# Kernel tuning notes

Measured on AMD Instinct MI355X. Metric: run time of the kernel, lower is better.

## Reference

```python
import jax, jax.numpy as jnp
import numpy as np

N_NODES = 100000
N_EDGES = 3200000
IN_DIM, BIG, HID = 4, 32, 2
EPS = 1e-5


def _lin_init(key, fan_in, fan_out):
    # torch nn.Linear default: U(-1/sqrt(fan_in), 1/sqrt(fan_in))
    kw, kb = jax.random.split(key)
    bound = 1.0 / np.sqrt(fan_in)
    w = jax.random.uniform(kw, (fan_in, fan_out), minval=-bound, maxval=bound, dtype=jnp.float32)
    b = jax.random.uniform(kb, (fan_out,), minval=-bound, maxval=bound, dtype=jnp.float32)
    return w, b


def setup_inputs() -> dict:
    key = jax.random.key(0)
    ks = jax.random.split(key, 9)
    x = jax.random.normal(ks[0], (N_NODES, IN_DIM), dtype=jnp.float32)
    edge_index = jax.random.randint(ks[1], (2, N_EDGES), 0, N_NODES, dtype=jnp.int32)
    bn_w = jnp.ones((IN_DIM,), jnp.float32)
    bn_b = jnp.zeros((IN_DIM,), jnp.float32)
    enc_w1, enc_b1 = _lin_init(ks[2], 2 * IN_DIM, BIG)
    enc_w2, enc_b2 = _lin_init(ks[3], BIG, BIG)
    enc_w3, enc_b3 = _lin_init(ks[4], BIG, HID)
    dec_w1, dec_b1 = _lin_init(ks[5], 2 * HID, BIG)
    dec_w2, dec_b2 = _lin_init(ks[6], BIG, BIG)
    dec_w3, dec_b3 = _lin_init(ks[7], BIG, IN_DIM)
    return dict(x=x, edge_index=edge_index, bn_w=bn_w, bn_b=bn_b,
                enc_w1=enc_w1, enc_b1=enc_b1, enc_w2=enc_w2, enc_b2=enc_b2,
                enc_w3=enc_w3, enc_b3=enc_b3,
                dec_w1=dec_w1, dec_b1=dec_b1, dec_w2=dec_w2, dec_b2=dec_b2,
                dec_w3=dec_w3, dec_b3=dec_b3)


def _edge_conv(x, src, dst, w1, b1, w2, b2, w3, b3, final_relu):
    # PyG EdgeConv: message = nn(cat([x_i, x_j - x_i])), mean-aggregated at target i (=dst)
    xi = x[dst]                     # [E, F] gather (target)
    xj = x[src]                     # [E, F] gather (source)
    h = jnp.concatenate([xi, xj - xi], axis=-1)  # [E, 2F]
    h = jax.nn.relu(h @ w1 + b1)
    h = jax.nn.relu(h @ w2 + b2)
    h = h @ w3 + b3
    if final_relu:
        h = jax.nn.relu(h)
    n = x.shape[0]
    agg = jax.ops.segment_sum(h, dst, num_segments=n)          # [N, out]
    cnt = jax.ops.segment_sum(jnp.ones((h.shape[0],), h.dtype), dst, num_segments=n)
    return agg / jnp.maximum(cnt, 1.0)[:, None]


def reference(x, edge_index, bn_w, bn_b,
              enc_w1, enc_b1, enc_w2, enc_b2, enc_w3, enc_b3,
              dec_w1, dec_b1, dec_w2, dec_b2, dec_w3, dec_b3):
    # BatchNorm1d (training mode: batch statistics, biased variance)
    mu = jnp.mean(x, axis=0)
    var = jnp.var(x, axis=0)
    h = (x - mu) * jax.lax.rsqrt(var + EPS) * bn_w + bn_b
    src, dst = edge_index[0], edge_index[1]
    h = _edge_conv(h, src, dst, enc_w1, enc_b1, enc_w2, enc_b2, enc_w3, enc_b3, final_relu=True)
    h = _edge_conv(h, src, dst, dec_w1, dec_b1, dec_w2, dec_b2, dec_w3, dec_b3, final_relu=False)
    return h
```

## Files before the change

kernel.cpp:

```cpp
#include <hip/hip_runtime.h>

#define N_NODES 100000
#define N_EDGES 3200000
#define EPS 1e-5f
#define NODE_BLOCKS 391
#define NB 782
#define BSTRIDE 4608
#define NSUB 9
#define S1_EPB 8192
#define S1_BLOCKS 391

typedef unsigned int uint;
typedef uint u32x4 __attribute__((ext_vector_type(4)));
typedef _Float16 f16x8 __attribute__((ext_vector_type(8)));
typedef _Float16 f16x2 __attribute__((ext_vector_type(2)));
typedef float f32x16 __attribute__((ext_vector_type(16)));

static __device__ __forceinline__ f16x8 as_h8(u32x4 u) { return __builtin_bit_cast(f16x8, u); }
static __device__ __forceinline__ uint pkh(float a, float b) {
    return __builtin_bit_cast(uint, __builtin_amdgcn_cvt_pkrtz(a, b));
}
static __device__ __forceinline__ void swap32(uint& a, uint& b) {
    asm volatile("v_permlane32_swap_b32 %0, %1" : "+v"(a), "+v"(b));
}
static __device__ __forceinline__ uint prelu(uint u, uint z) {
    uint r;
    asm("v_pk_max_f16 %0, %1, %2" : "=v"(r) : "v"(u), "v"(z));
    return r;
}

#define MFMA(A, B, C) __builtin_amdgcn_mfma_f32_32x32x16_f16(as_h8(A), as_h8(B), (C), 0, 0, 0)

static __device__ __forceinline__ void repack(const f32x16& c, u32x4& f0, u32x4& f1, uint z) {
    uint p0 = prelu(pkh(c[0], c[1]), z),   p1 = prelu(pkh(c[2], c[3]), z);
    uint q0 = prelu(pkh(c[4], c[5]), z),   q1 = prelu(pkh(c[6], c[7]), z);
    uint p2 = prelu(pkh(c[8], c[9]), z),   p3 = prelu(pkh(c[10], c[11]), z);
    uint q2 = prelu(pkh(c[12], c[13]), z), q3 = prelu(pkh(c[14], c[15]), z);
    swap32(p0, q0); swap32(p1, q1);
    swap32(p2, q2); swap32(p3, q3);
    f0.x = p0; f0.y = p1; f0.z = q0; f0.w = q1;
    f1.x = p2; f1.y = p3; f1.z = q2; f1.w = q3;
}

#define OFF_STATS  0
#define OFF_BCNT   1024
#define OFF_INVCNT 5120
#define OFF_AGG1   405120
#define OFF_DECW   1205120
#define OFF_BUCKET 1214848
#define OFF_PENC   15629696
#define OFF_PCNT   22836608
#define OFF_PDEC   26440064
#define OFF_ENCW   26440064


__global__ __launch_bounds__(256) void k_bn_stats(const float* __restrict__ x,
                                                  double* __restrict__ stats) {
    int i = blockIdx.x * 256 + threadIdx.x;
    float4 v = make_float4(0.f, 0.f, 0.f, 0.f);
    if (i < N_NODES) v = ((const float4*)x)[i];
    double a[8];
    a[0] = v.x; a[1] = v.y; a[2] = v.z; a[3] = v.w;
    a[4] = (double)v.x * v.x; a[5] = (double)v.y * v.y;
    a[6] = (double)v.z * v.z; a[7] = (double)v.w * v.w;
    #pragma unroll
    for (int off = 32; off > 0; off >>= 1) {
        #pragma unroll
        for (int j = 0; j < 8; j++) a[j] += __shfl_down(a[j], off);
    }
    __shared__ double smem[4][8];
    int wave = threadIdx.x >> 6;
    int lane = threadIdx.x & 63;
    if (lane == 0) {
        #pragma unroll
        for (int j = 0; j < 8; j++) smem[wave][j] = a[j];
    }
    __syncthreads();
    if (threadIdx.x == 0) {
        #pragma unroll
        for (int j = 0; j < 8; j++) {
            double t = smem[0][j] + smem[1][j] + smem[2][j] + smem[3][j];
            atomicAdd(&stats[j], t);
        }
    }
}

static __device__ __forceinline__ uint pk_part(float a, float b, int part) {
    _Float16 ah = (_Float16)a, bh = (_Float16)b;
    if (part) {
        a -= (float)ah; b -= (float)bh;
        ah = (_Float16)a; bh = (_Float16)b;
    }
    return (uint)__builtin_bit_cast(unsigned short, ah) |
           ((uint)__builtin_bit_cast(unsigned short, bh) << 16);
}

__global__ __launch_bounds__(256) void k_prep(const double* __restrict__ stats,
                                              const float* __restrict__ bn_w,
                                              const float* __restrict__ bn_b,
                                              const float* __restrict__ ew1,
                                              const float* __restrict__ eb1,
                                              const float* __restrict__ ew2,
                                              const float* __restrict__ eb2,
                                              const float* __restrict__ ew3,
                                              const float* __restrict__ eb3,
                                              const float* __restrict__ dw1,
                                              const float* __restrict__ db1,
                                              const float* __restrict__ dw2,
                                              const float* __restrict__ db2,
                                              const float* __restrict__ dw3,
                                              const float* __restrict__ db3,
                                              uint* __restrict__ encw,
                                              uint* __restrict__ decw) {
    int t = threadIdx.x;
    int lane = t >> 2, d = t & 3;
    int hi = lane >> 5, m = lane & 31;

    const double inv_n = 1.0 / (double)N_NODES;
    float sc[4], sh[4];
    #pragma unroll
    for (int dd = 0; dd < 4; dd++) {
        double mu = stats[dd] * inv_n;
        double vr = stats[4 + dd] * inv_n - mu * mu;
        float rs = (float)(1.0 / sqrt(vr + (double)EPS));
        sc[dd] = rs * bn_w[dd];
        sh[dd] = bn_b[dd] - (float)mu * sc[dd];
    }

    {
        int j = 2 * d;
        float a = ew1[j * 32 + m] * sc[j & 3];
        float bb = ew1[(j + 1) * 32 + m] * sc[(j + 1) & 3];
        encw[t] = pk_part(a, bb, hi);
    }
    {
        int j = 2 * d;
        float a = (j < 4) ? dw1[j * 32 + m] : 0.f;
        float bb = (j + 1 < 4) ? dw1[(j + 1) * 32 + m] : 0.f;
        decw[t] = pk_part(a, bb, hi);
    }
    #pragma unroll
    for (int tile = 0; tile < 2; tile++) {
        int k = 16 * tile + 8 * hi + 2 * d;
        {
            float a = ew2[k * 32 + m], bb = ew2[(k + 1) * 32 + m];
            encw[256 + tile * 256 + t] = pk_part(a, bb, 0);
            encw[768 + tile * 256 + t] = pk_part(a, bb, 1);
        }
        {
            float a = dw2[k * 32 + m], bb = dw2[(k + 1) * 32 + m];
            decw[256 + tile * 256 + t] = pk_part(a, bb, 0);
            decw[768 + tile * 256 + t] = pk_part(a, bb, 1);
        }
        {
            float a = (m < 2) ? ew3[k * 2 + m] : 0.f;
            float bb = (m < 2) ? ew3[(k + 1) * 2 + m] : 0.f;
            encw[1280 + tile * 256 + t] = pk_part(a, bb, 0);
            encw[1792 + tile * 256 + t] = pk_part(a, bb, 1);
        }
        {
            float a = (m < 4) ? dw3[k * 4 + m] : 0.f;
            float bb = (m < 4) ? dw3[(k + 1) * 4 + m] : 0.f;
            decw[1280 + tile * 256 + t] = pk_part(a, bb, 0);
            decw[1792 + tile * 256 + t] = pk_part(a, bb, 1);
        }
    }
    if (t < 32) {
        int hh = t >> 4, r = t & 15;
        int row = (r & 3) + 8 * (r >> 2) + 4 * hh;
        float b1p = eb1[row];
        #pragma unroll
        for (int dd = 0; dd < 4; dd++) b1p += ew1[dd * 32 + row] * sh[dd];
        ((float*)encw)[2304 + t] = b1p;
        ((float*)encw)[2336 + t] = eb2[row];
        ((float*)encw)[2368 + t] = (row < 2) ? eb3[row] : 0.f;
        ((float*)decw)[2304 + t] = db1[row];
        ((float*)decw)[2336 + t] = db2[row];
        ((float*)decw)[2368 + t] = (row < 4) ? db3[row] : 0.f;
    }
}

__global__ __launch_bounds__(256) void k_s1(const int* __restrict__ ei,
                                            int* __restrict__ bcnt,
                                            int* __restrict__ bucket_buf) {
    __shared__ int hist[NB];
    __shared__ int base[NB];
    __shared__ int run[NB];
    __shared__ int gbase[NB];
    __shared__ int entries[S1_EPB];
    __shared__ unsigned short bk16[S1_EPB];
    __shared__ int wsum[4];
    int tid = threadIdx.x;
    int e0 = blockIdx.x * S1_EPB;
    for (int i = tid; i < NB; i += 256) hist[i] = 0;
    __syncthreads();
    #pragma unroll
    for (int k = 0; k < 32; k++) {
        int e = e0 + k * 256 + tid;
        if (e < N_EDGES) atomicAdd(&hist[ei[N_EDGES + e] >> 7], 1);
    }
    __syncthreads();
    int t4 = tid * 4;
    int h0 = (t4 + 0 < NB) ? hist[t4 + 0] : 0;
    int h1 = (t4 + 1 < NB) ? hist[t4 + 1] : 0;
    int h2 = (t4 + 2 < NB) ? hist[t4 + 2] : 0;
    int h3 = (t4 + 3 < NB) ? hist[t4 + 3] : 0;
    int tsum = h0 + h1 + h2 + h3;
    int lane = tid & 63, wv = tid >> 6;
    int xs = tsum;
    #pragma unroll
    for (int off = 1; off < 64; off <<= 1) {
        int u = __shfl_up(xs, off);
        if (lane >= off) xs += u;
    }
    if (lane == 63) wsum[wv] = xs;
    __syncthreads();
    int wo = 0;
    #pragma unroll
    for (int w = 0; w < 4; w++) if (w < wv) wo += wsum[w];
    int texcl = wo + xs - tsum;
    if (t4 + 0 < NB) base[t4 + 0] = texcl;
    if (t4 + 1 < NB) base[t4 + 1] = texcl + h0;
    if (t4 + 2 < NB) base[t4 + 2] = texcl + h0 + h1;
    if (t4 + 3 < NB) base[t4 + 3] = texcl + h0 + h1 + h2;
    __syncthreads();
    for (int i = tid; i < NB; i += 256) {
        int h = hist[i];
        gbase[i] = i * BSTRIDE + (h ? atomicAdd(&bcnt[i], h) : 0);
        run[i] = base[i];
    }
    __syncthreads();
    #pragma unroll
    for (int k = 0; k < 32; k++) {
        int e = e0 + k * 256 + tid;
        if (e < N_EDGES) {
            int s = ei[e];
            int d = ei[N_EDGES + e];
            int b = d >> 7;
            int r = atomicAdd(&run[b], 1);
            entries[r] = s | ((d & 127) << 17);
            bk16[r] = (unsigned short)b;
        }
    }
    __syncthreads();
    int nloc = min(S1_EPB, N_EDGES - e0);
    for (int idx = tid; idx < nloc; idx += 256) {
        int b = bk16[idx];
        bucket_buf[gbase[b] + (idx - base[b])] = entries[idx];
    }
}

__global__ __launch_bounds__(256, 3) void k_enc_partial(const float* __restrict__ x,
                                                        const int* __restrict__ bucket_buf,
                                                        const int* __restrict__ bcnt,
                                                        float2* __restrict__ penc,
                                                        int* __restrict__ pcnt,
                                                        const uint* __restrict__ encw) {
    __shared__ float4 xs[128];
    __shared__ float acc0[128], acc1[128];
    __shared__ int lc[128];
    int b = blockIdx.x, sub = blockIdx.y, tid = threadIdx.x;
    int lane = tid & 63, hi = lane >> 5, col = lane & 31, wv = tid >> 6;
    int cb = bcnt[b];
    int node0 = b << 7;

    if (tid < 128) {
        acc0[tid] = 0.f; acc1[tid] = 0.f; lc[tid] = 0;
        int n = node0 + tid;
        if (n >= N_NODES) n = 0;
        xs[tid] = ((const float4*)x)[n];
    }
    __syncthreads();

    const u32x4* W4 = (const u32x4*)encw;
    u32x4 w1   = W4[lane];
    u32x4 w2h0 = W4[64 + lane],  w2h1 = W4[128 + lane];
    u32x4 w2l0 = W4[192 + lane], w2l1 = W4[256 + lane];
    u32x4 u3h0 = W4[320 + lane], u3h1 = W4[384 + lane];
    u32x4 u3l0 = W4[448 + lane], u3l1 = W4[512 + lane];
    const float* tf = (const float*)encw;
    f32x16 b1f, b2f, b3f;
    {
        const float4* p1 = (const float4*)(tf + 2304 + hi * 16);
        const float4* p2 = (const float4*)(tf + 2336 + hi * 16);
        const float4* p3 = (const float4*)(tf + 2368 + hi * 16);
        #pragma unroll
        for (int q = 0; q < 4; q++) {
            float4 a = p1[q], c = p2[q], e = p3[q];
            b1f[4 * q] = a.x; b1f[4 * q + 1] = a.y; b1f[4 * q + 2] = a.z; b1f[4 * q + 3] = a.w;
            b2f[4 * q] = c.x; b2f[4 * q + 1] = c.y; b2f[4 * q + 2] = c.z; b2f[4 * q + 3] = c.w;
            b3f[4 * q] = e.x; b3f[4 * q + 1] = e.y; b3f[4 * q + 2] = e.z; b3f[4 * q + 3] = e.w;
        }
    }
    uint z = 0;

    if (sub * 512 < cb) {
        int sbase = sub * 512 + col * 16 + wv * 4;
        int4 q = *(const int4*)&bucket_buf[b * BSTRIDE + sbase];
        int ents[4] = {q.x, q.y, q.z, q.w};
        int ss[4], ia[4];
        #pragma unroll
        for (int t = 0; t < 4; t++) {
            int s = ents[t] & 0x1FFFF;
            if (s >= N_NODES) s = 0;
            ss[t] = s;
            ia[t] = (ents[t] >> 17) & 127;
        }
        float4 xj[4];
        #pragma unroll
        for (int t = 0; t < 4; t++) xj[t] = ((const float4*)x)[ss[t]];

        #pragma unroll
        for (int t = 0; t < 4; t++) {
            float4 xi = xs[ia[t]];
            u32x4 xf;
            xf.x = pkh(xi.x, xi.y);
            xf.y = pkh(xi.z, xi.w);
            xf.z = pkh(xj[t].x - xi.x, xj[t].y - xi.y);
            xf.w = pkh(xj[t].z - xi.z, xj[t].w - xi.w);
            f32x16 c = MFMA(w1, xf, b1f);
            u32x4 f0, f1;
            repack(c, f0, f1, z);
            f32x16 c2 = MFMA(w2h0, f0, b2f);
            c2 = MFMA(w2h1, f1, c2);
            c2 = MFMA(w2l0, f0, c2);
            c2 = MFMA(w2l1, f1, c2);
            u32x4 e0, e1;
            repack(c2, e0, e1, z);
            f32x16 c3 = MFMA(u3h0, e0, b3f);
            c3 = MFMA(u3h1, e1, c3);
            c3 = MFMA(u3l0, e0, c3);
            c3 = MFMA(u3l1, e1, c3);
            if (hi == 0 && (sbase + t) < cb) {
                float o0 = fmaxf(c3[0], 0.f);
                float o1 = fmaxf(c3[1], 0.f);
                atomicAdd(&acc0[ia[t]], o0);
                atomicAdd(&acc1[ia[t]], o1);
                atomicAdd(&lc[ia[t]], 1);
            }
        }
    }
    __syncthreads();
    if (tid < 128) {
        int pb = b * NSUB + sub;
        penc[pb * 128 + tid] = make_float2(acc0[tid], acc1[tid]);
        pcnt[pb * 128 + tid] = lc[tid];
    }
}

__global__ __launch_bounds__(256) void k_reduce_enc_p(const float2* __restrict__ penc,
                                                      const int* __restrict__ pcnt,
                                                      float2* __restrict__ agg1,
                                                      float* __restrict__ invcnt) {
    int i = blockIdx.x * 256 + threadIdx.x;
    if (i >= N_NODES) return;
    int b = i >> 7, l = i & 127;
    float a0 = 0.f, a1 = 0.f;
    int c = 0;
    #pragma unroll
    for (int sub = 0; sub < NSUB; sub++) {
        int idx = (b * NSUB + sub) * 128 + l;
        float2 p = penc[idx];
        a0 += p.x; a1 += p.y;
        c += pcnt[idx];
    }
    float ic = 1.0f / (float)(c > 1 ? c : 1);
    invcnt[i] = ic;
    agg1[i] = make_float2(a0 * ic, a1 * ic);
}

__global__ __launch_bounds__(256, 3) void k_dec_partial(const float2* __restrict__ henc,
                                                        const int* __restrict__ bucket_buf,
                                                        const int* __restrict__ bcnt,
                                                        float4* __restrict__ pdec,
                                                        const uint* __restrict__ decw) {
    __shared__ float2 hld[128];
    __shared__ float a0s[128], a1s[128], a2s[128], a3s[128];
    int b = blockIdx.x, sub = blockIdx.y, tid = threadIdx.x;
    int lane = tid & 63, hi = lane >> 5, col = lane & 31, wv = tid >> 6;
    int cb = bcnt[b];
    int node0 = b << 7;

    if (tid < 128) {
        a0s[tid] = 0.f; a1s[tid] = 0.f; a2s[tid] = 0.f; a3s[tid] = 0.f;
        int n = node0 + tid;
        if (n >= N_NODES) n = 0;
        hld[tid] = henc[n];
    }
    __syncthreads();

    const u32x4* W4 = (const u32x4*)decw;
    u32x4 v1   = W4[lane];
    u32x4 v2h0 = W4[64 + lane],  v2h1 = W4[128 + lane];
    u32x4 v2l0 = W4[192 + lane], v2l1 = W4[256 + lane];
    u32x4 u3h0 = W4[320 + lane], u3h1 = W4[384 + lane];
    u32x4 u3l0 = W4[448 + lane], u3l1 = W4[512 + lane];
    const float* tf = (const float*)decw;
    f32x16 b1f, b2f, b3f;
    {
        const float4* p1 = (const float4*)(tf + 2304 + hi * 16);
        const float4* p2 = (const float4*)(tf + 2336 + hi * 16);
        const float4* p3 = (const float4*)(tf + 2368 + hi * 16);
        #pragma unroll
        for (int q = 0; q < 4; q++) {
            float4 a = p1[q], c = p2[q], e = p3[q];
            b1f[4 * q] = a.x; b1f[4 * q + 1] = a.y; b1f[4 * q + 2] = a.z; b1f[4 * q + 3] = a.w;
            b2f[4 * q] = c.x; b2f[4 * q + 1] = c.y; b2f[4 * q + 2] = c.z; b2f[4 * q + 3] = c.w;
            b3f[4 * q] = e.x; b3f[4 * q + 1] = e.y; b3f[4 * q + 2] = e.z; b3f[4 * q + 3] = e.w;
        }
    }
    uint z = 0;

    if (sub * 512 < cb) {
        int sbase = sub * 512 + col * 16 + wv * 4;
        int4 q = *(const int4*)&bucket_buf[b * BSTRIDE + sbase];
        int ents[4] = {q.x, q.y, q.z, q.w};
        int ss[4], ia[4];
        #pragma unroll
        for (int t = 0; t < 4; t++) {
            int s = ents[t] & 0x1FFFF;
            if (s >= N_NODES) s = 0;
            ss[t] = s;
            ia[t] = (ents[t] >> 17) & 127;
        }
        float2 hj[4], hiv[4];
        #pragma unroll
        for (int t = 0; t < 4; t++) hj[t] = henc[ss[t]];
        #pragma unroll
        for (int t = 0; t < 4; t++) hiv[t] = hld[ia[t]];

        #pragma unroll
        for (int t = 0; t < 4; t++) {
            u32x4 xf;
            xf.x = pkh(hiv[t].x, hiv[t].y);
            xf.y = pkh(hj[t].x - hiv[t].x, hj[t].y - hiv[t].y);
            xf.z = 0u; xf.w = 0u;
            f32x16 c = MFMA(v1, xf, b1f);
            u32x4 f0, f1;
            repack(c, f0, f1, z);
            f32x16 c2 = MFMA(v2h0, f0, b2f);
            c2 = MFMA(v2h1, f1, c2);
            c2 = MFMA(v2l0, f0, c2);
            c2 = MFMA(v2l1, f1, c2);
            u32x4 e0, e1;
            repack(c2, e0, e1, z);
            f32x16 c3 = MFMA(u3h0, e0, b3f);
            c3 = MFMA(u3h1, e1, c3);
            c3 = MFMA(u3l0, e0, c3);
            c3 = MFMA(u3l1, e1, c3);
            if (hi == 0 && (sbase + t) < cb) {
                atomicAdd(&a0s[ia[t]], c3[0]);
                atomicAdd(&a1s[ia[t]], c3[1]);
                atomicAdd(&a2s[ia[t]], c3[2]);
                atomicAdd(&a3s[ia[t]], c3[3]);
            }
        }
    }
    __syncthreads();
    if (tid < 128) {
        int pb = b * NSUB + sub;
        pdec[pb * 128 + tid] = make_float4(a0s[tid], a1s[tid], a2s[tid], a3s[tid]);
    }
}

__global__ __launch_bounds__(256) void k_reduce_dec_p(const float4* __restrict__ pdec,
                                                      const float* __restrict__ invcnt,
                                                      float4* __restrict__ out) {
    int i = blockIdx.x * 256 + threadIdx.x;
    if (i >= N_NODES) return;
    int b = i >> 7, l = i & 127;
    float a0 = 0.f, a1 = 0.f, a2 = 0.f, a3 = 0.f;
    #pragma unroll
    for (int sub = 0; sub < NSUB; sub++) {
        float4 p = pdec[(b * NSUB + sub) * 128 + l];
        a0 += p.x; a1 += p.y; a2 += p.z; a3 += p.w;
    }
    float ic = invcnt[i];
    out[i] = make_float4(a0 * ic, a1 * ic, a2 * ic, a3 * ic);
}

extern "C" void kernel_launch(void* const* d_in, const int* in_sizes, int n_in,
                              void* d_out, int out_size, void* d_ws, size_t ws_size,
                              hipStream_t stream) {
    const float* x    = (const float*)d_in[0];
    const int*   ei   = (const int*)d_in[1];
    const float* bn_w = (const float*)d_in[2];
    const float* bn_b = (const float*)d_in[3];
    const float* ew1  = (const float*)d_in[4];
    const float* eb1  = (const float*)d_in[5];
    const float* ew2  = (const float*)d_in[6];
    const float* eb2  = (const float*)d_in[7];
    const float* ew3  = (const float*)d_in[8];
    const float* eb3  = (const float*)d_in[9];
    const float* dw1  = (const float*)d_in[10];
    const float* db1  = (const float*)d_in[11];
    const float* dw2  = (const float*)d_in[12];
    const float* db2  = (const float*)d_in[13];
    const float* dw3  = (const float*)d_in[14];
    const float* db3  = (const float*)d_in[15];

    char* ws = (char*)d_ws;
    double* stats      = (double*)(ws + OFF_STATS);
    int*    bcnt       = (int*)(ws + OFF_BCNT);
    float*  invcnt     = (float*)(ws + OFF_INVCNT);
    float2* agg1       = (float2*)(ws + OFF_AGG1);
    uint*   decw       = (uint*)(ws + OFF_DECW);
    int*    bucket_buf = (int*)(ws + OFF_BUCKET);
    float2* penc       = (float2*)(ws + OFF_PENC);
    int*    pcnt       = (int*)(ws + OFF_PCNT);
    float4* pdec       = (float4*)(ws + OFF_PDEC);
    uint*   encw       = (uint*)(ws + OFF_ENCW);
    float4* out        = (float4*)d_out;

    hipMemsetAsync(ws, 0, 5120, stream);

    k_bn_stats<<<NODE_BLOCKS, 256, 0, stream>>>(x, stats);
    k_prep<<<1, 256, 0, stream>>>(stats, bn_w, bn_b, ew1, eb1, ew2, eb2, ew3, eb3,
                                  dw1, db1, dw2, db2, dw3, db3, encw, decw);
    k_s1<<<S1_BLOCKS, 256, 0, stream>>>(ei, bcnt, bucket_buf);
    k_enc_partial<<<dim3(NB, NSUB), 256, 0, stream>>>(x, bucket_buf, bcnt,
                                                      penc, pcnt, encw);
    k_reduce_enc_p<<<NODE_BLOCKS, 256, 0, stream>>>(penc, pcnt, agg1, invcnt);
    k_dec_partial<<<dim3(NB, NSUB), 256, 0, stream>>>(agg1, bucket_buf, bcnt, pdec, decw);
    k_reduce_dec_p<<<NODE_BLOCKS, 256, 0, stream>>>(pdec, invcnt, out);
}
```

Before: 305.9 us.

## Halve layer-3 MFMAs via split output rows and process three edge windows per wave

Layer-3 weights are repacked so the output channels are spread across both half-waves, which cuts the final projection from four MFMAs to two per edge. Bias is folded in by subtracting b2 and adding a per-lane constant. Each half-wave now does its own atomics into separate accumulators. Sub-blocks drop from 9 to 3, and each wave handles three 512-edge windows, prefetching the next window's gathers before computing the current one, to hide gather latency and amortise block setup. The cost is fewer blocks in flight and more registers per thread.

```diff
diff --git a/kernel.cpp b/kernel.cpp
--- a/kernel.cpp
+++ b/kernel.cpp
@@ -6,14 +6,13 @@
 #define NODE_BLOCKS 391
 #define NB 782
 #define BSTRIDE 4608
-#define NSUB 9
+#define NSUB 3
 #define S1_EPB 8192
 #define S1_BLOCKS 391
 
 typedef unsigned int uint;
 typedef uint u32x4 __attribute__((ext_vector_type(4)));
 typedef _Float16 f16x8 __attribute__((ext_vector_type(8)));
-typedef _Float16 f16x2 __attribute__((ext_vector_type(2)));
 typedef float f32x16 __attribute__((ext_vector_type(16)));
 
 static __device__ __forceinline__ f16x8 as_h8(u32x4 u) { return __builtin_bit_cast(f16x8, u); }
@@ -40,6 +39,17 @@
     swap32(p2, q2); swap32(p3, q3);
     f0.x = p0; f0.y = p1; f0.z = q0; f0.w = q1;
     f1.x = p2; f1.y = p3; f1.z = q2; f1.w = q3;
+}
+
+static __device__ __forceinline__ void decode4(const int4& q, int* ss, int* ia) {
+    int e0 = q.x, e1 = q.y, e2 = q.z, e3 = q.w;
+    ss[0] = e0 & 0x1FFFF; ia[0] = (e0 >> 17) & 127;
+    ss[1] = e1 & 0x1FFFF; ia[1] = (e1 >> 17) & 127;
+    ss[2] = e2 & 0x1FFFF; ia[2] = (e2 >> 17) & 127;
+    ss[3] = e3 & 0x1FFFF; ia[3] = (e3 >> 17) & 127;
+    #pragma unroll
+    for (int k = 0; k < 4; k++)
+        if (ss[k] >= N_NODES) ss[k] = 0;
 }
 
 #define OFF_STATS  0
@@ -153,16 +163,20 @@
             decw[768 + tile * 256 + t] = pk_part(a, bb, 1);
         }
         {
-            float a = (m < 2) ? ew3[k * 2 + m] : 0.f;
-            float bb = (m < 2) ? ew3[(k + 1) * 2 + m] : 0.f;
+            float a = 0.f, bb = 0.f;
+            if (m == 0 || m == 4) {
+                int o = m >> 2;
+                a = ew3[k * 2 + o]; bb = ew3[(k + 1) * 2 + o];
+            }
             encw[1280 + tile * 256 + t] = pk_part(a, bb, 0);
-            encw[1792 + tile * 256 + t] = pk_part(a, bb, 1);
         }
         {
-            float a = (m < 4) ? dw3[k * 4 + m] : 0.f;
-            float bb = (m < 4) ? dw3[(k + 1) * 4 + m] : 0.f;
+            float a = 0.f, bb = 0.f;
+            if ((m & 3) < 2 && m < 6) {
+                int o = (m & 1) + 2 * (m >> 2);
+                a = dw3[k * 4 + o]; bb = dw3[(k + 1) * 4 + o];
+            }
             decw[1280 + tile * 256 + t] = pk_part(a, bb, 0);
-            decw[1792 + tile * 256 + t] = pk_part(a, bb, 1);
         }
     }
     if (t < 32) {
@@ -171,12 +185,13 @@
         float b1p = eb1[row];
         #pragma unroll
         for (int dd = 0; dd < 4; dd++) b1p += ew1[dd * 32 + row] * sh[dd];
-        ((float*)encw)[2304 + t] = b1p;
-        ((float*)encw)[2336 + t] = eb2[row];
-        ((float*)encw)[2368 + t] = (row < 2) ? eb3[row] : 0.f;
-        ((float*)decw)[2304 + t] = db1[row];
-        ((float*)decw)[2336 + t] = db2[row];
-        ((float*)decw)[2368 + t] = (row < 4) ? db3[row] : 0.f;
+        ((float*)encw)[1792 + t] = b1p;
+        ((float*)encw)[1824 + t] = eb2[row];
+        ((float*)encw)[1856 + t] = (row == 0) ? eb3[0] : (row == 4) ? eb3[1] : 0.f;
+        ((float*)decw)[1792 + t] = db1[row];
+        ((float*)decw)[1824 + t] = db2[row];
+        ((float*)decw)[1856 + t] =
+            ((row & 3) < 2 && row < 6) ? db3[(row & 1) + 2 * (row >> 2)] : 0.f;
     }
 }
 
@@ -276,69 +291,79 @@
     u32x4 w1   = W4[lane];
     u32x4 w2h0 = W4[64 + lane],  w2h1 = W4[128 + lane];
     u32x4 w2l0 = W4[192 + lane], w2l1 = W4[256 + lane];
-    u32x4 u3h0 = W4[320 + lane], u3h1 = W4[384 + lane];
-    u32x4 u3l0 = W4[448 + lane], u3l1 = W4[512 + lane];
+    u32x4 w30  = W4[320 + lane], w31  = W4[384 + lane];
     const float* tf = (const float*)encw;
-    f32x16 b1f, b2f, b3f;
+    f32x16 b1f, b2f;
     {
-        const float4* p1 = (const float4*)(tf + 2304 + hi * 16);
-        const float4* p2 = (const float4*)(tf + 2336 + hi * 16);
-        const float4* p3 = (const float4*)(tf + 2368 + hi * 16);
+        const float4* p1 = (const float4*)(tf + 1792 + hi * 16);
+        const float4* p2 = (const float4*)(tf + 1824 + hi * 16);
         #pragma unroll
         for (int q = 0; q < 4; q++) {
-            float4 a = p1[q], c = p2[q], e = p3[q];
+            float4 a = p1[q], c = p2[q];
             b1f[4 * q] = a.x; b1f[4 * q + 1] = a.y; b1f[4 * q + 2] = a.z; b1f[4 * q + 3] = a.w;
             b2f[4 * q] = c.x; b2f[4 * q + 1] = c.y; b2f[4 * q + 2] = c.z; b2f[4 * q + 3] = c.w;
-            b3f[4 * q] = e.x; b3f[4 * q + 1] = e.y; b3f[4 * q + 2] = e.z; b3f[4 * q + 3] = e.w;
-        }
-    }
+        }
+    }
+    float bc0 = tf[1856 + hi * 16] - b2f[0];
+    float* accH = hi ? acc1 : acc0;
     uint z = 0;
 
-    if (sub * 512 < cb) {
-        int sbase = sub * 512 + col * 16 + wv * 4;
-        int4 q = *(const int4*)&bucket_buf[b * BSTRIDE + sbase];
-        int ents[4] = {q.x, q.y, q.z, q.w};
-        int ss[4], ia[4];
-        #pragma unroll
-        for (int t = 0; t < 4; t++) {
-            int s = ents[t] & 0x1FFFF;
-            if (s >= N_NODES) s = 0;
-            ss[t] = s;
-            ia[t] = (ents[t] >> 17) & 127;
-        }
-        float4 xj[4];
-        #pragma unroll
-        for (int t = 0; t < 4; t++) xj[t] = ((const float4*)x)[ss[t]];
-
-        #pragma unroll
-        for (int t = 0; t < 4; t++) {
-            float4 xi = xs[ia[t]];
-            u32x4 xf;
-            xf.x = pkh(xi.x, xi.y);
-            xf.y = pkh(xi.z, xi.w);
-            xf.z = pkh(xj[t].x - xi.x, xj[t].y - xi.y);
-            xf.w = pkh(xj[t].z - xi.z, xj[t].w - xi.w);
-            f32x16 c = MFMA(w1, xf, b1f);
-            u32x4 f0, f1;
-            repack(c, f0, f1, z);
-            f32x16 c2 = MFMA(w2h0, f0, b2f);
-            c2 = MFMA(w2h1, f1, c2);
-            c2 = MFMA(w2l0, f0, c2);
-            c2 = MFMA(w2l1, f1, c2);
-            u32x4 e0, e1;
-            repack(c2, e0, e1, z);
-            f32x16 c3 = MFMA(u3h0, e0, b3f);
-            c3 = MFMA(u3h1, e1, c3);
-            c3 = MFMA(u3l0, e0, c3);
-            c3 = MFMA(u3l1, e1, c3);
-            if (hi == 0 && (sbase + t) < cb) {
-                float o0 = fmaxf(c3[0], 0.f);
-                float o1 = fmaxf(c3[1], 0.f);
-                atomicAdd(&acc0[ia[t]], o0);
-                atomicAdd(&acc1[ia[t]], o1);
-                atomicAdd(&lc[ia[t]], 1);
+    int wb0 = sub * 1536 + wv * 128;
+    if (wb0 < cb) {
+        const int4* BB = (const int4*)&bucket_buf[b * BSTRIDE];
+        int i0 = (wb0 >> 2) + col;
+        int4 qa = BB[i0];
+        int4 qb = BB[i0 + 128];
+        int4 qc = BB[i0 + 256];
+        bool act1 = (wb0 + 512) < cb;
+        bool act2 = (wb0 + 1024) < cb;
+
+        auto enc_win = [&](const int* ia, const float4* xg, int wb) {
+            #pragma unroll
+            for (int j = 0; j < 4; j++) {
+                float4 xi = xs[ia[j]];
+                u32x4 xf;
+                xf.x = pkh(xi.x, xi.y);
+                xf.y = pkh(xi.z, xi.w);
+                xf.z = pkh(xg[j].x - xi.x, xg[j].y - xi.y);
+                xf.w = pkh(xg[j].z - xi.z, xg[j].w - xi.w);
+                f32x16 c = MFMA(w1, xf, b1f);
+                u32x4 f0, f1;
+                repack(c, f0, f1, z);
+                f32x16 c2 = MFMA(w2h0, f0, b2f);
+                c2 = MFMA(w2h1, f1, c2);
+                c2 = MFMA(w2l0, f0, c2);
+                c2 = MFMA(w2l1, f1, c2);
+                u32x4 e0, e1;
+                repack(c2, e0, e1, z);
+                f32x16 c3 = MFMA(w30, e0, b2f);
+                c3 = MFMA(w31, e1, c3);
+                float o = fmaxf(c3[0] + bc0, 0.f);
+                if ((wb + col * 4 + j) < cb) {
+                    atomicAdd(&accH[ia[j]], o);
+                    if (hi == 0) atomicAdd(&lc[ia[j]], 1);
+                }
             }
-        }
+        };
+
+        int s0[4], s1[4], s2[4], ia0[4], ia1[4], ia2[4];
+        float4 xg0[4], xg1[4], xg2[4];
+        decode4(qa, s0, ia0);
+        #pragma unroll
+        for (int k = 0; k < 4; k++) xg0[k] = ((const float4*)x)[s0[k]];
+        if (act1) {
+            decode4(qb, s1, ia1);
+            #pragma unroll
+            for (int k = 0; k < 4; k++) xg1[k] = ((const float4*)x)[s1[k]];
+        }
+        enc_win(ia0, xg0, wb0);
+        if (act2) {
+            decode4(qc, s2, ia2);
+            #pragma unroll
+            for (int k = 0; k < 4; k++) xg2[k] = ((const float4*)x)[s2[k]];
+        }
+        if (act1) enc_win(ia1, xg1, wb0 + 512);
+        if (act2) enc_win(ia2, xg2, wb0 + 1024);
     }
     __syncthreads();
     if (tid < 128) {
@@ -393,68 +418,81 @@
     u32x4 v1   = W4[lane];
     u32x4 v2h0 = W4[64 + lane],  v2h1 = W4[128 + lane];
     u32x4 v2l0 = W4[192 + lane], v2l1 = W4[256 + lane];
-    u32x4 u3h0 = W4[320 + lane], u3h1 = W4[384 + lane];
-    u32x4 u3l0 = W4[448 + lane], u3l1 = W4[512 + lane];
+    u32x4 w30  = W4[320 + lane], w31  = W4[384 + lane];
     const float* tf = (const float*)decw;
-    f32x16 b1f, b2f, b3f;
+    f32x16 b1f, b2f;
     {
-        const float4* p1 = (const float4*)(tf + 2304 + hi * 16);
-        const float4* p2 = (const float4*)(tf + 2336 + hi * 16);
-        const float4* p3 = (const float4*)(tf + 2368 + hi * 16);
+        const float4* p1 = (const float4*)(tf + 1792 + hi * 16);
+        const float4* p2 = (const float4*)(tf + 1824 + hi * 16);
         #pragma unroll
         for (int q = 0; q < 4; q++) {
-            float4 a = p1[q], c = p2[q], e = p3[q];
+            float4 a = p1[q], c = p2[q];
             b1f[4 * q] = a.x; b1f[4 * q + 1] = a.y; b1f[4 * q + 2] = a.z; b1f[4 * q + 3] = a.w;
             b2f[4 * q] = c.x; b2f[4 * q + 1] = c.y; b2f[4 * q + 2] = c.z; b2f[4 * q + 3] = c.w;
-            b3f[4 * q] = e.x; b3f[4 * q + 1] = e.y; b3f[4 * q + 2] = e.z; b3f[4 * q + 3] = e.w;
-        }
-    }
+        }
+    }
+    float bc0 = tf[1856 + hi * 16 + 0] - b2f[0];
+    float bc1 = tf[1856 + hi * 16 + 1] - b2f[1];
+    float* accA = hi ? a2s : a0s;
+    float* accB = hi ? a3s : a1s;
     uint z = 0;
 
-    if (sub * 512 < cb) {
-        int sbase = sub * 512 + col * 16 + wv * 4;
-        int4 q = *(const int4*)&bucket_buf[b * BSTRIDE + sbase];
-        int ents[4] = {q.x, q.y, q.z, q.w};
-        int ss[4], ia[4];
-        #pragma unroll
-        for (int t = 0; t < 4; t++) {
-            int s = ents[t] & 0x1FFFF;
-            if (s >= N_NODES) s = 0;
-            ss[t] = s;
-            ia[t] = (ents[t] >> 17) & 127;
-        }
-        float2 hj[4], hiv[4];
-        #pragma unroll
-        for (int t = 0; t < 4; t++) hj[t] = henc[ss[t]];
-        #pragma unroll
-        for (int t = 0; t < 4; t++) hiv[t] = hld[ia[t]];
-
-        #pragma unroll
-        for (int t = 0; t < 4; t++) {
-            u32x4 xf;
-            xf.x = pkh(hiv[t].x, hiv[t].y);
-            xf.y = pkh(hj[t].x - hiv[t].x, hj[t].y - hiv[t].y);
-            xf.z = 0u; xf.w = 0u;
-            f32x16 c = MFMA(v1, xf, b1f);
-            u32x4 f0, f1;
-            repack(c, f0, f1, z);
-            f32x16 c2 = MFMA(v2h0, f0, b2f);
-            c2 = MFMA(v2h1, f1, c2);
-            c2 = MFMA(v2l0, f0, c2);
-            c2 = MFMA(v2l1, f1, c2);
-            u32x4 e0, e1;
-            repack(c2, e0, e1, z);
-            f32x16 c3 = MFMA(u3h0, e0, b3f);
-            c3 = MFMA(u3h1, e1, c3);
-            c3 = MFMA(u3l0, e0, c3);
-            c3 = MFMA(u3l1, e1, c3);
-            if (hi == 0 && (sbase + t) < cb) {
-                atomicAdd(&a0s[ia[t]], c3[0]);
-                atomicAdd(&a1s[ia[t]], c3[1]);
-                atomicAdd(&a2s[ia[t]], c3[2]);
-                atomicAdd(&a3s[ia[t]], c3[3]);
+    int wb0 = sub * 1536 + wv * 128;
+    if (wb0 < cb) {
+        const int4* BB = (const int4*)&bucket_buf[b * BSTRIDE];
+        int i0 = (wb0 >> 2) + col;
+        int4 qa = BB[i0];
+        int4 qb = BB[i0 + 128];
+        int4 qc = BB[i0 + 256];
+        bool act1 = (wb0 + 512) < cb;
+        bool act2 = (wb0 + 1024) < cb;
+
+        auto dec_win = [&](const int* ia, const float2* hj, int wb) {
+            #pragma unroll
+            for (int j = 0; j < 4; j++) {
+                float2 h2 = hld[ia[j]];
+                u32x4 xf;
+                xf.x = pkh(h2.x, h2.y);
+                xf.y = pkh(hj[j].x - h2.x, hj[j].y - h2.y);
+                xf.z = 0u; xf.w = 0u;
+                f32x16 c = MFMA(v1, xf, b1f);
+                u32x4 f0, f1;
+                repack(c, f0, f1, z);
+                f32x16 c2 = MFMA(v2h0, f0, b2f);
+                c2 = MFMA(v2h1, f1, c2);
+                c2 = MFMA(v2l0, f0, c2);
+                c2 = MFMA(v2l1, f1, c2);
+                u32x4 e0, e1;
+                repack(c2, e0, e1, z);
+                f32x16 c3 = MFMA(w30, e0, b2f);
+                c3 = MFMA(w31, e1, c3);
+                float o0 = c3[0] + bc0;
+                float o1 = c3[1] + bc1;
+                if ((wb + col * 4 + j) < cb) {
+                    atomicAdd(&accA[ia[j]], o0);
+                    atomicAdd(&accB[ia[j]], o1);
+                }
             }
-        }
+        };
+
+        int s0[4], s1[4], s2[4], ia0[4], ia1[4], ia2[4];
+        float2 hg0[4], hg1[4], hg2[4];
+        decode4(qa, s0, ia0);
+        #pragma unroll
+        for (int k = 0; k < 4; k++) hg0[k] = henc[s0[k]];
+        if (act1) {
+            decode4(qb, s1, ia1);
+            #pragma unroll
+            for (int k = 0; k < 4; k++) hg1[k] = henc[s1[k]];
+        }
+        dec_win(ia0, hg0, wb0);
+        if (act2) {
+            decode4(qc, s2, ia2);
+            #pragma unroll
+            for (int k = 0; k < 4; k++) hg2[k] = henc[s2[k]];
+        }
+        if (act1) dec_win(ia1, hg1, wb0 + 512);
+        if (act2) dec_win(ia2, hg2, wb0 + 1024);
     }
     __syncthreads();
     if (tid < 128) {
```

Result: no change. 305.4 us (-0.2%).
